# Optimization experiments

Hardware: AMD Instinct MI355X
Metric: run time of the kernel (lower is better)

The kernel has to match this reference:

```python
import jax, jax.numpy as jnp
import numpy as np

SEQ = 4096
D_EMB = 2048
D_HEAD = 128
SCALE = 0.02


def setup_inputs() -> dict:
    key = jax.random.key(0)
    kx, kq, kk, kv, ko = jax.random.split(key, 5)
    x = jax.random.normal(kx, (SEQ, D_EMB), dtype=jnp.float32)
    W_Q = jax.random.normal(kq, (D_EMB, D_EMB), dtype=jnp.float32) * SCALE
    W_K = jax.random.normal(kk, (D_EMB, D_EMB), dtype=jnp.float32) * SCALE
    W_V = jax.random.normal(kv, (D_EMB, D_EMB), dtype=jnp.float32) * SCALE
    W_O = jax.random.normal(ko, (D_EMB, D_EMB), dtype=jnp.float32) * SCALE
    b_Q = jnp.zeros((D_EMB,), dtype=jnp.float32)
    b_K = jnp.zeros((D_EMB,), dtype=jnp.float32)
    b_V = jnp.zeros((D_EMB,), dtype=jnp.float32)
    b_O = jnp.zeros((D_EMB,), dtype=jnp.float32)
    return {"x": x, "W_Q": W_Q, "W_K": W_K, "W_V": W_V, "W_O": W_O,
            "b_Q": b_Q, "b_K": b_K, "b_V": b_V, "b_O": b_O, "d_head": D_HEAD}


def reference(x, W_Q, W_K, W_V, W_O, b_Q, b_K, b_V, b_O, d_head):
    # x: [S, D]
    q = x @ W_Q + b_Q  # [S, D]
    k = x @ W_K + b_K
    v = x @ W_V + b_V
    scores = (q @ k.T) / jnp.sqrt(jnp.float32(d_head))  # [S, S]
    seq = scores.shape[0]
    causal = jnp.tril(jnp.ones((seq, seq), dtype=bool))
    scores = jnp.where(causal, scores, -jnp.inf)
    weights = jax.nn.softmax(scores, axis=-1)  # [S, S]
    attn_out = weights @ v  # [S, D]
    return attn_out @ W_O + b_O
```

## Files before the change

### kernel.cpp

```cpp
#include <hip/hip_runtime.h>
#include <hip/hip_fp16.h>

typedef _Float16 f16;
typedef _Float16 f16x8 __attribute__((ext_vector_type(8)));
typedef _Float16 f16x4 __attribute__((ext_vector_type(4)));
typedef float    f32x4 __attribute__((ext_vector_type(4)));

#define SEQ      4096
#define DEMB     2048
#define SCALE_QK 0.08838834764831845f

#define GAS __attribute__((address_space(1)))
#define LAS __attribute__((address_space(3)))

__device__ __forceinline__ void load_lds16(const f16* g, f16* l) {
    __builtin_amdgcn_global_load_lds((const GAS void*)g, (LAS void*)l, 16, 0, 0);
}

__device__ __forceinline__ f16x8 ldsr(const f16* base, int byteoff) {
    byteoff ^= (byteoff >> 3) & 0x70;
    return *(const f16x8*)((const char*)base + byteoff);
}

__device__ __forceinline__ void stage_half(const f16* __restrict__ src, int ldk,
                                           f16* ldsdst, int tid) {
#pragma unroll
    for (int s = 0; s < 2; ++s) {
        const int o   = s * 8192 + tid * 16;
        const int osw = o ^ ((o >> 3) & 0x70);
        load_lds16(src + (size_t)(osw >> 7) * ldk + ((osw & 127) >> 1),
                   ldsdst + (s * 8192 + (tid >> 6) * 1024) / 2);
    }
}

template <int MODE>
__device__ __forceinline__ void gemm_core(
        const f16* __restrict__ A, int lda, const f16* __restrict__ BT, int ldb,
        void* __restrict__ outp, int ldo, const float* __restrict__ bias,
        int bm, int bn, int NI, int kt0, float scale, f16* lds, int roff) {
    const int m0 = bm * 256, n0 = bn * 256;

    const int tid  = threadIdx.x;
    const int lane = tid & 63;
    const int wr   = (tid >> 6) >> 2;
    const int wc   = (tid >> 6) & 3;
    const int fr   = lane & 15;
    const int kb   = (lane >> 4) * 16;

    const f16* Abase = A + (size_t)m0 * lda + kt0 * 64;
    const f16* Bbase = BT + (size_t)n0 * ldb + kt0 * 64;

#define STG(buf, isB, half, t) \
    stage_half((isB) ? (Bbase + (size_t)((half) * 128) * ldb + (t) * 64) \
                     : (Abase + (size_t)((half) * 128) * lda + (t) * 64), \
               (isB) ? ldb : lda, \
               lds + (buf) * 32768 + (isB) * 16384 + (half) * 8192, tid)

    f32x4 acc[8][4] = {};
    f16x8 af[8], bf0[4], bf1[4];

#define READ_A(Mh, buf) { \
    const f16* bb = lds + (buf) * 32768; \
    _Pragma("unroll") for (int m = 0; m < 4; ++m) \
    _Pragma("unroll") for (int ks = 0; ks < 2; ++ks) \
        af[m * 2 + ks] = ldsr(bb, ((Mh) * 128 + wr * 64 + m * 16 + fr) * 128 + ks * 64 + kb); }

#define READ_B(Nh, buf, dst) { \
    const f16* bb = lds + (buf) * 32768 + 16384; \
    _Pragma("unroll") for (int n = 0; n < 2; ++n) \
    _Pragma("unroll") for (int ks = 0; ks < 2; ++ks) \
        dst[n * 2 + ks] = ldsr(bb, ((Nh) * 128 + wc * 32 + n * 16 + fr) * 128 + ks * 64 + kb); }

#define MFMA_PH(Mh, Nh, bfx) { \
    __builtin_amdgcn_s_setprio(1); \
    _Pragma("unroll") for (int m = 0; m < 4; ++m) \
    _Pragma("unroll") for (int n = 0; n < 2; ++n) \
    _Pragma("unroll") for (int ks = 0; ks < 2; ++ks) \
        acc[(Mh) * 4 + m][(Nh) * 2 + n] = __builtin_amdgcn_mfma_f32_16x16x32_f16( \
            af[m * 2 + ks], bfx[n * 2 + ks], acc[(Mh) * 4 + m][(Nh) * 2 + n], 0, 0, 0); \
    __builtin_amdgcn_s_setprio(0); }

#define BAR   asm volatile("s_barrier" ::: "memory")
#define VM6   asm volatile("s_waitcnt vmcnt(6)" ::: "memory")
#define VM0   asm volatile("s_waitcnt vmcnt(0)" ::: "memory")

    STG(0, 0, 0, 0); STG(0, 1, 0, 0); STG(0, 1, 1, 0); STG(0, 0, 1, 0);
    STG(1, 0, 0, 1); STG(1, 1, 0, 1); STG(1, 1, 1, 1);
    VM6; BAR;

    for (int i = 0; i < NI; ++i) {
        const int t0 = 2 * i;
        const bool more = (i + 1 < NI);
        READ_A(0, 0); READ_B(0, 0, bf0);
        STG(1, 0, 1, t0 + 1);
        BAR; MFMA_PH(0, 0, bf0); BAR;
        READ_B(1, 0, bf1);
        if (more) STG(0, 0, 0, t0 + 2);
        BAR; MFMA_PH(0, 1, bf1); BAR;
        READ_A(1, 0);
        if (more) STG(0, 1, 0, t0 + 2);
        BAR; MFMA_PH(1, 0, bf0); BAR;
        if (more) { STG(0, 1, 1, t0 + 2); VM6; } else { VM0; }
        BAR; MFMA_PH(1, 1, bf1); BAR;
        READ_A(0, 1); READ_B(0, 1, bf0);
        if (more) STG(0, 0, 1, t0 + 2);
        BAR; MFMA_PH(0, 0, bf0); BAR;
        READ_B(1, 1, bf1);
        if (more) STG(1, 0, 0, t0 + 3);
        BAR; MFMA_PH(0, 1, bf1); BAR;
        READ_A(1, 1);
        if (more) STG(1, 1, 0, t0 + 3);
        BAR; MFMA_PH(1, 0, bf0); BAR;
        if (more) STG(1, 1, 1, t0 + 3);
        VM6;
        BAR; MFMA_PH(1, 1, bf1); BAR;
    }

    const int rq = (lane >> 4) * 4;
#pragma unroll
    for (int mi = 0; mi < 8; ++mi) {
        const int row = m0 + (mi >> 2) * 128 + wr * 64 + (mi & 3) * 16 + rq;
#pragma unroll
        for (int ni = 0; ni < 4; ++ni) {
            const int col = n0 + (ni >> 1) * 128 + wc * 32 + (ni & 1) * 16 + fr;
            if (MODE == 0) {
                f16* o = (f16*)outp;
                const float bv = bias[col];
#pragma unroll
                for (int r = 0; r < 4; ++r)
                    o[(size_t)(row + r) * ldo + col] = (f16)(acc[mi][ni][r] + bv);
            } else if (MODE == 1) {
                f16* o = (f16*)outp;
                f16x4 v;
#pragma unroll
                for (int r = 0; r < 4; ++r) v[r] = (f16)acc[mi][ni][r];
                *(f16x4*)&o[(size_t)col * ldo + row] = v;
            } else if (MODE == 2) {
                float* o = (float*)outp;
                if (bias) {
                    const float bv = bias[col];
#pragma unroll
                    for (int r = 0; r < 4; ++r)
                        o[(size_t)(row + r) * ldo + col] = acc[mi][ni][r] + bv;
                } else {
#pragma unroll
                    for (int r = 0; r < 4; ++r)
                        o[(size_t)(row - roff + r) * ldo + col] = acc[mi][ni][r];
                }
            } else {
                f16* o = (f16*)outp;
#pragma unroll
                for (int r = 0; r < 4; ++r)
                    o[(size_t)(row + r) * ldo + col] = (f16)(acc[mi][ni][r] * scale);
            }
        }
    }
#undef STG
#undef READ_A
#undef READ_B
#undef MFMA_PH
#undef BAR
#undef VM6
#undef VM0
}

__global__ __launch_bounds__(256) void k_prep(
        const float* __restrict__ x, const float* __restrict__ WV,
        const float* __restrict__ bQ, const float* __restrict__ bK,
        const float* __restrict__ bO,
        f16* __restrict__ x16, f16* __restrict__ wv16,
        float* __restrict__ bqk, float* __restrict__ bc) {
    const int bid = blockIdx.x;
    if (bid < 12288) {
        const bool isX = bid < 8192;
        const float* src = isX ? x : WV;
        f16* dst = isX ? x16 : wv16;
        const int i = (isX ? bid : bid - 8192) * 1024 + threadIdx.x * 4;
        float4 v = *(const float4*)&src[i];
        f16x4 o; o[0] = (f16)v.x; o[1] = (f16)v.y; o[2] = (f16)v.z; o[3] = (f16)v.w;
        *(f16x4*)&dst[i] = o;
    } else if (bid < 12292) {
        const int i = (bid - 12288) * 1024 + threadIdx.x * 4;
        float4 v = (i < 2048) ? *(const float4*)&bQ[i]
                              : *(const float4*)&bK[i - 2048];
        *(float4*)&bqk[i] = v;
    } else {
        const int i = (bid - 12292) * 1024 + threadIdx.x * 4;
        *(float4*)&bc[i] = *(const float4*)&bO[i];
    }
}

__global__ __launch_bounds__(256) void transpose_cvt3(
        const float* __restrict__ WQ, const float* __restrict__ WK,
        const float* __restrict__ WO,
        f16* __restrict__ wqkt, f16* __restrict__ wot) {
    __shared__ f16 tile[64][72];
    const int z = blockIdx.z;
    const float* in = z == 0 ? WQ : z == 1 ? WK : WO;
    f16* out = z == 0 ? wqkt : z == 1 ? wqkt + (size_t)DEMB * DEMB : wot;
    const int c0 = blockIdx.x * 64, r0 = blockIdx.y * 64;
    const int tx = threadIdx.x & 63, ty = threadIdx.x >> 6;
    for (int rr = ty; rr < 64; rr += 4)
        tile[tx][rr] = (f16)in[(size_t)(r0 + rr) * DEMB + c0 + tx];
    __syncthreads();
    for (int cc = ty; cc < 64; cc += 4)
        out[(size_t)(c0 + cc) * DEMB + r0 + tx] = tile[cc][tx];
}

__global__ __launch_bounds__(512, 2)
void k_mix1(const f16* __restrict__ x16, const f16* __restrict__ wqkt,
            f16* __restrict__ qk16, const float* __restrict__ bqk,
            const f16* __restrict__ wv16, const f16* __restrict__ wot,
            f16* __restrict__ wvoT, const float* __restrict__ WO,
            const float* __restrict__ bV, float* __restrict__ bc) {
    __shared__ f16 lds[65536];
    const int bid = blockIdx.x;
    if (bid < 128) {
        gemm_core<0>(x16, DEMB, wqkt, DEMB, qk16, 2 * DEMB, bqk,
                     bid >> 4, bid & 15, 16, 0, 1.f, lds, 0);
    } else if (bid < 192) {
        const int w = bid - 128;
        gemm_core<1>(wv16, DEMB, wot, DEMB, wvoT, DEMB, nullptr,
                     w >> 3, w & 7, 16, 0, 1.f, lds, 0);
    } else {
        const int b  = bid - 192;
        const int j0 = (b & 7) * 256;
        const int i0 = (b >> 3) * 256 + (threadIdx.x >> 8) * 128;
        const int jj = threadIdx.x & 255;
        float acc = 0.f;
        for (int i = i0; i < i0 + 128; ++i)
            acc += bV[i] * WO[(size_t)i * DEMB + j0 + jj];
        atomicAdd(&bc[j0 + jj], acc);
    }
}

__global__ __launch_bounds__(512, 2)
void k_mix2(const f16* __restrict__ x16, const f16* __restrict__ wqkt,
            f16* __restrict__ qk16, const float* __restrict__ bqk,
            const f16* __restrict__ wvoT, f16* __restrict__ vwT) {
    __shared__ f16 lds[65536];
    const int bid = blockIdx.x;
    if (bid < 128) {
        gemm_core<0>(x16, DEMB, wqkt, DEMB, qk16, 2 * DEMB, bqk,
                     8 + (bid >> 4), bid & 15, 16, 0, 1.f, lds, 0);
    } else {
        const int b = bid - 128;
        gemm_core<1>(x16, DEMB, wvoT, DEMB, vwT, SEQ, nullptr,
                     b >> 3, b & 7, 16, 0, 1.f, lds, 0);
    }
}

__global__ __launch_bounds__(512, 2)
void k_scores(const f16* __restrict__ qk16, f16* __restrict__ sb) {
    __shared__ f16 lds[65536];
    const int bid = blockIdx.x;
    int bm = (int)((sqrtf(8.f * bid + 1.f) - 1.f) * 0.5f);
    while ((bm + 1) * (bm + 2) / 2 <= bid) ++bm;
    while (bm * (bm + 1) / 2 > bid) --bm;
    const int bn = bid - bm * (bm + 1) / 2;
    gemm_core<3>(qk16, 2 * DEMB, qk16 + DEMB, 2 * DEMB, sb, SEQ, nullptr,
                 bm, bn, 16, 0, SCALE_QK, lds, 0);
}

__global__ __launch_bounds__(256) void k_softmax(f16* __restrict__ sb) {
    __shared__ f16 srow[SEQ];
    __shared__ float red[8];
    const int i  = blockIdx.x;
    const int L  = i + 1;
    const int Lp = ((i >> 8) + 1) << 8;
    f16* row = sb + (size_t)i * SEQ;
    const int t = threadIdx.x;

    float mx = -3.0e38f;
    for (int j0 = t * 8; j0 < Lp; j0 += 2048) {
        f16x8 v = *(const f16x8*)&row[j0];
        *(f16x8*)&srow[j0] = v;
#pragma unroll
        for (int u = 0; u < 8; ++u)
            if (j0 + u < L) mx = fmaxf(mx, (float)v[u]);
    }
#pragma unroll
    for (int o = 32; o > 0; o >>= 1) mx = fmaxf(mx, __shfl_xor(mx, o));
    if ((t & 63) == 0) red[t >> 6] = mx;
    __syncthreads();
    mx = fmaxf(fmaxf(red[0], red[1]), fmaxf(red[2], red[3]));

    float sm = 0.f;
    for (int j0 = t * 8; j0 < Lp; j0 += 2048) {
        f16x8 v = *(const f16x8*)&srow[j0];
#pragma unroll
        for (int u = 0; u < 8; ++u)
            if (j0 + u < L) sm += __expf((float)v[u] - mx);
    }
#pragma unroll
    for (int o = 32; o > 0; o >>= 1) sm += __shfl_xor(sm, o);
    if ((t & 63) == 0) red[4 + (t >> 6)] = sm;
    __syncthreads();
    const float inv = 1.f / (red[4] + red[5] + red[6] + red[7]);

    for (int j0 = t * 8; j0 < Lp; j0 += 2048) {
        f16x8 v = *(const f16x8*)&srow[j0];
        f16x8 wv;
#pragma unroll
        for (int u = 0; u < 8; ++u)
            wv[u] = (j0 + u < L) ? (f16)(__expf((float)v[u] - mx) * inv) : (f16)0.f;
        *(f16x8*)&row[j0] = wv;
    }
}

__global__ __launch_bounds__(512, 2)
void k_pvw(const f16* __restrict__ sb, const f16* __restrict__ vwT,
           float* __restrict__ out, const float* __restrict__ bc,
           float* __restrict__ part1, float* __restrict__ part2) {
    __shared__ f16 lds[65536];
    static const short BMt[30] = {0,1,2,3,4,5,6,6,7,7,8,8,9,9,10,10,11,11,
                                  12,12,12,13,13,13,14,14,14,15,15,15};
    static const short KT0t[30] = {0,0,0,0,0,0,0,14,0,16,0,18,0,20,0,22,0,24,
                                   0,18,36,0,20,38,0,20,40,0,22,44};
    static const short NIt[30] = {2,4,6,8,10,12,7,7,8,8,9,9,10,10,11,11,12,12,
                                  9,9,8,10,9,9,10,10,10,11,11,10};
    static const short ORDt[30] = {0,0,0,0,0,0,0,1,0,1,0,1,0,1,0,1,0,1,
                                   0,1,2,0,1,2,0,1,2,0,1,2};
    const int e = blockIdx.x, bn = blockIdx.y;
    const int bm = BMt[e], kt0 = KT0t[e], ni = NIt[e], ord = ORDt[e];
    float* op = ord == 0 ? out : ord == 1 ? part1 : part2;
    const int roff = ord == 1 ? 1536 : 3072;
    gemm_core<2>(sb, SEQ, vwT, SEQ, op, DEMB, ord == 0 ? bc : nullptr,
                 bm, bn, ni, kt0, 1.f, lds, roff);
}

__global__ __launch_bounds__(256) void k_reduce(
        float* __restrict__ out, const float* __restrict__ part1,
        const float* __restrict__ part2) {
    const int idx = (blockIdx.x * 256 + threadIdx.x) * 4;
    float4 o = *(float4*)&out[(size_t)1536 * DEMB + idx];
    float4 p = *(const float4*)&part1[idx];
    o.x += p.x; o.y += p.y; o.z += p.z; o.w += p.w;
    if (idx >= 1536 * DEMB) {
        float4 q = *(const float4*)&part2[idx - 1536 * DEMB];
        o.x += q.x; o.y += q.y; o.z += q.z; o.w += q.w;
    }
    *(float4*)&out[(size_t)1536 * DEMB + idx] = o;
}

extern "C" void kernel_launch(void* const* d_in, const int* in_sizes, int n_in,
                              void* d_out, int out_size, void* d_ws, size_t ws_size,
                              hipStream_t stream) {
    const float* x  = (const float*)d_in[0];
    const float* WQ = (const float*)d_in[1];
    const float* WK = (const float*)d_in[2];
    const float* WV = (const float*)d_in[3];
    const float* WO = (const float*)d_in[4];
    const float* bQ = (const float*)d_in[5];
    const float* bK = (const float*)d_in[6];
    const float* bV = (const float*)d_in[7];
    const float* bO = (const float*)d_in[8];
    float* out = (float*)d_out;

    char* w = (char*)d_ws;
    f16* qk16 = (f16*)w; w += (size_t)SEQ * 2 * DEMB * 2;
    f16* sb   = (f16*)w; w += (size_t)SEQ * SEQ * 2;
    f16* x16  = (f16*)w; w += (size_t)SEQ * DEMB * 2;
    f16* wqkt = (f16*)w; w += (size_t)2 * DEMB * DEMB * 2;
    f16* wv16 = (f16*)w; w += (size_t)DEMB * DEMB * 2;
    f16* wot  = (f16*)w; w += (size_t)DEMB * DEMB * 2;
    f16* wvoT = (f16*)w; w += (size_t)DEMB * DEMB * 2;
    float* bqk = (float*)w; w += 2 * DEMB * 4;
    float* bc  = (float*)w; w += DEMB * 4 + 4096;
    f16* vwT = wv16;
    float* part1 = (float*)qk16;
    float* part2 = (float*)qk16 + (size_t)2560 * DEMB;

    k_prep<<<12294, 256, 0, stream>>>(x, WV, bQ, bK, bO, x16, wv16, bqk, bc);
    transpose_cvt3<<<dim3(DEMB / 64, DEMB / 64, 3), 256, 0, stream>>>(
        WQ, WK, WO, wqkt, wot);

    k_mix1<<<256, 512, 0, stream>>>(x16, wqkt, qk16, bqk, wv16, wot, wvoT,
                                    WO, bV, bc);

    k_mix2<<<256, 512, 0, stream>>>(x16, wqkt, qk16, bqk, wvoT, vwT);

    k_scores<<<136, 512, 0, stream>>>(qk16, sb);

    k_softmax<<<SEQ, 256, 0, stream>>>(sb);

    k_pvw<<<dim3(30, 8), 512, 0, stream>>>(sb, vwT, out, bc, part1, part2);

    k_reduce<<<5120, 256, 0, stream>>>(out, part1, part2);
}
```

Baseline: 286.4 us.

## Fold weight transpose into prep kernel and rebalance causal PV split-K partition

The separate transpose/convert kernel for W_Q, W_K and W_O is merged into k_prep as extra blocks, removing one kernel launch and letting the two conversion jobs share a single grid. The causal PV×W GEMM partition table grows from 30 to 32 work entries per column block, giving 256 blocks. Row blocks from 5 upward now split over K, and the partial-sum rows start at 1280 and 2816. part2 is moved into the now-unused wqkt buffer, and k_reduce is widened to cover the larger partial region. This costs more reduction traffic in exchange for a more even per-block workload on the triangular attention matrix.

```diff
diff --git a/kernel.cpp b/kernel.cpp
--- a/kernel.cpp
+++ b/kernel.cpp
@@ -166,10 +166,14 @@
 
 __global__ __launch_bounds__(256) void k_prep(
         const float* __restrict__ x, const float* __restrict__ WV,
+        const float* __restrict__ WQ, const float* __restrict__ WK,
+        const float* __restrict__ WO,
         const float* __restrict__ bQ, const float* __restrict__ bK,
         const float* __restrict__ bO,
         f16* __restrict__ x16, f16* __restrict__ wv16,
+        f16* __restrict__ wqkt, f16* __restrict__ wot,
         float* __restrict__ bqk, float* __restrict__ bc) {
+    __shared__ f16 tile[64][72];
     const int bid = blockIdx.x;
     if (bid < 12288) {
         const bool isX = bid < 8192;
@@ -179,26 +183,26 @@
         float4 v = *(const float4*)&src[i];
         f16x4 o; o[0] = (f16)v.x; o[1] = (f16)v.y; o[2] = (f16)v.z; o[3] = (f16)v.w;
         *(f16x4*)&dst[i] = o;
-    } else if (bid < 12292) {
+        return;
+    }
+    if (bid < 12292) {
         const int i = (bid - 12288) * 1024 + threadIdx.x * 4;
         float4 v = (i < 2048) ? *(const float4*)&bQ[i]
                               : *(const float4*)&bK[i - 2048];
         *(float4*)&bqk[i] = v;
-    } else {
+        return;
+    }
+    if (bid < 12294) {
         const int i = (bid - 12292) * 1024 + threadIdx.x * 4;
         *(float4*)&bc[i] = *(const float4*)&bO[i];
-    }
-}
-
-__global__ __launch_bounds__(256) void transpose_cvt3(
-        const float* __restrict__ WQ, const float* __restrict__ WK,
-        const float* __restrict__ WO,
-        f16* __restrict__ wqkt, f16* __restrict__ wot) {
-    __shared__ f16 tile[64][72];
-    const int z = blockIdx.z;
+        return;
+    }
+    const int b = bid - 12294;
+    const int z = b >> 10;
+    const int rem = b & 1023;
     const float* in = z == 0 ? WQ : z == 1 ? WK : WO;
     f16* out = z == 0 ? wqkt : z == 1 ? wqkt + (size_t)DEMB * DEMB : wot;
-    const int c0 = blockIdx.x * 64, r0 = blockIdx.y * 64;
+    const int c0 = (rem & 31) * 64, r0 = (rem >> 5) * 64;
     const int tx = threadIdx.x & 63, ty = threadIdx.x >> 6;
     for (int rr = ty; rr < 64; rr += 4)
         tile[tx][rr] = (f16)in[(size_t)(r0 + rr) * DEMB + c0 + tx];
@@ -313,18 +317,21 @@
            float* __restrict__ out, const float* __restrict__ bc,
            float* __restrict__ part1, float* __restrict__ part2) {
     __shared__ f16 lds[65536];
-    static const short BMt[30] = {0,1,2,3,4,5,6,6,7,7,8,8,9,9,10,10,11,11,
-                                  12,12,12,13,13,13,14,14,14,15,15,15};
-    static const short KT0t[30] = {0,0,0,0,0,0,0,14,0,16,0,18,0,20,0,22,0,24,
-                                   0,18,36,0,20,38,0,20,40,0,22,44};
-    static const short NIt[30] = {2,4,6,8,10,12,7,7,8,8,9,9,10,10,11,11,12,12,
-                                  9,9,8,10,9,9,10,10,10,11,11,10};
-    static const short ORDt[30] = {0,0,0,0,0,0,0,1,0,1,0,1,0,1,0,1,0,1,
-                                   0,1,2,0,1,2,0,1,2,0,1,2};
+    static const short BMt[32]  = {0,1,2,3,4, 5,5, 6,6, 7,7, 8,8, 9,9, 10,10,
+                                   11,11,11, 12,12,12, 13,13,13, 14,14,14,
+                                   15,15,15};
+    static const short KT0t[32] = {0,0,0,0,0, 0,12, 0,14, 0,16, 0,18, 0,20,
+                                   0,22, 0,16,32, 0,18,36, 0,20,38, 0,20,40,
+                                   0,22,44};
+    static const short NIt[32]  = {2,4,6,8,10, 6,6, 7,7, 8,8, 9,9, 10,10,
+                                   11,11, 8,8,8, 9,9,8, 10,9,9, 10,10,10,
+                                   11,11,10};
+    static const short ORDt[32] = {0,0,0,0,0, 0,1, 0,1, 0,1, 0,1, 0,1, 0,1,
+                                   0,1,2, 0,1,2, 0,1,2, 0,1,2, 0,1,2};
     const int e = blockIdx.x, bn = blockIdx.y;
     const int bm = BMt[e], kt0 = KT0t[e], ni = NIt[e], ord = ORDt[e];
     float* op = ord == 0 ? out : ord == 1 ? part1 : part2;
-    const int roff = ord == 1 ? 1536 : 3072;
+    const int roff = ord == 1 ? 1280 : 2816;
     gemm_core<2>(sb, SEQ, vwT, SEQ, op, DEMB, ord == 0 ? bc : nullptr,
                  bm, bn, ni, kt0, 1.f, lds, roff);
 }
@@ -333,14 +340,14 @@
         float* __restrict__ out, const float* __restrict__ part1,
         const float* __restrict__ part2) {
     const int idx = (blockIdx.x * 256 + threadIdx.x) * 4;
-    float4 o = *(float4*)&out[(size_t)1536 * DEMB + idx];
+    float4 o = *(float4*)&out[(size_t)1280 * DEMB + idx];
     float4 p = *(const float4*)&part1[idx];
     o.x += p.x; o.y += p.y; o.z += p.z; o.w += p.w;
     if (idx >= 1536 * DEMB) {
         float4 q = *(const float4*)&part2[idx - 1536 * DEMB];
         o.x += q.x; o.y += q.y; o.z += q.z; o.w += q.w;
     }
-    *(float4*)&out[(size_t)1536 * DEMB + idx] = o;
+    *(float4*)&out[(size_t)1280 * DEMB + idx] = o;
 }
 
 extern "C" void kernel_launch(void* const* d_in, const int* in_sizes, int n_in,
@@ -369,11 +376,10 @@
     float* bc  = (float*)w; w += DEMB * 4 + 4096;
     f16* vwT = wv16;
     float* part1 = (float*)qk16;
-    float* part2 = (float*)qk16 + (size_t)2560 * DEMB;
-
-    k_prep<<<12294, 256, 0, stream>>>(x, WV, bQ, bK, bO, x16, wv16, bqk, bc);
-    transpose_cvt3<<<dim3(DEMB / 64, DEMB / 64, 3), 256, 0, stream>>>(
-        WQ, WK, WO, wqkt, wot);
+    float* part2 = (float*)wqkt;
+
+    k_prep<<<15366, 256, 0, stream>>>(x, WV, WQ, WK, WO, bQ, bK, bO,
+                                      x16, wv16, wqkt, wot, bqk, bc);
 
     k_mix1<<<256, 512, 0, stream>>>(x16, wqkt, qk16, bqk, wv16, wot, wvoT,
                                     WO, bV, bc);
@@ -384,7 +390,7 @@
 
     k_softmax<<<SEQ, 256, 0, stream>>>(sb);
 
-    k_pvw<<<dim3(30, 8), 512, 0, stream>>>(sb, vwT, out, bc, part1, part2);
-
-    k_reduce<<<5120, 256, 0, stream>>>(out, part1, part2);
-}
+    k_pvw<<<dim3(32, 8), 512, 0, stream>>>(sb, vwT, out, bc, part1, part2);
+
+    k_reduce<<<5632, 256, 0, stream>>>(out, part1, part2);
+}
```

Result: faster. 280.0 us (-2.2%).
